# Optimization experiments

Measured on AMD Instinct MI355X. Metric: run time of the kernel, lower is better.

Reference implementation:

```python
import jax, jax.numpy as jnp
import numpy as np
import math

# Dimensions (see shape_source)
B, C, NH = 4, 256, 8
VP, VW = 6, 16   # vertical: patches-per-window (outer), windows (inner)
HP, HW = 32, 3   # horizontal: patches-per-window (outer), windows (inner)
NW, P = VW * HW, VP * HP   # 48 windows, 192 patches per window
GRID = 96                   # patch grid is 96x96
SHIFT = (HP // 2, VP // 2)  # (16, 3) = (window_shape[0]//2, window_shape[1]//2)
FF = 4 * C
SCALE = 1.0 / math.sqrt(C)  # source divides by sqrt(embedding_dim), not head_dim


def setup_inputs() -> dict:
    key = jax.random.key(0)
    ks = jax.random.split(key, 17)
    std = 0.02
    n = lambda k, s: (jax.random.normal(k, s, dtype=jnp.float32) * std)
    return {
        "embeddings": jax.random.normal(ks[0], (B, GRID, GRID, C), dtype=jnp.float32),
        "ln1_g": jnp.ones((C,), jnp.float32), "ln1_b": jnp.zeros((C,), jnp.float32),
        "wq": n(ks[1], (C, C)), "bq": jnp.zeros((C,), jnp.float32),
        "wk": n(ks[2], (C, C)), "bk": jnp.zeros((C,), jnp.float32),
        "wv": n(ks[3], (C, C)), "bv": jnp.zeros((C,), jnp.float32),
        "pos_bias": n(ks[4], (NH, P, P)),
        "ln2_g": jnp.ones((C,), jnp.float32), "ln2_b": jnp.zeros((C,), jnp.float32),
        "w1": n(ks[5], (C, FF)), "b1": jnp.zeros((FF,), jnp.float32),
        "w2": n(ks[6], (FF, C)), "b2": jnp.zeros((C,), jnp.float32),
    }


def _ln(x, g, b, eps=1e-5):
    m = jnp.mean(x, axis=-1, keepdims=True)
    v = jnp.mean(jnp.square(x - m), axis=-1, keepdims=True)
    return (x - m) * jax.lax.rsqrt(v + eps) * g + b


def reference(embeddings, ln1_g, ln1_b, wq, bq, wk, bk, wv, bv, pos_bias,
              ln2_g, ln2_b, w1, b1, w2, b2):
    x = jnp.roll(embeddings, SHIFT, axis=(1, 2))
    # part: H=(VP outer, VW inner), W=(HP outer, HW inner) -> [B, NW, P, C]
    p = x.reshape(B, VP, VW, HP, HW, C).transpose(0, 2, 4, 1, 3, 5).reshape(B, NW, P, C)
    y = _ln(p, ln1_g, ln1_b)
    def heads(w, b):
        return (y @ w + b).reshape(B, NW, P, NH, C // NH).transpose(0, 1, 3, 2, 4)
    q, k, v = heads(wq, bq), heads(wk, bk), heads(wv, bv)  # [B, NW, NH, P, Dh]
    logits = jnp.einsum('bwhpd,bwhqd->bwhpq', q, k) * SCALE + pos_bias
    attn = jax.nn.softmax(logits, axis=-1)
    sa = jnp.einsum('bwhpq,bwhqd->bwhpd', attn, v)
    sa = sa.transpose(0, 1, 3, 2, 4).reshape(B, NW, P, C)
    a = p + sa
    h = _ln(a, ln2_g, ln2_b)
    ff = jax.nn.gelu(h @ w1 + b1, approximate=False) @ w2 + b2
    out = a + ff
    # join: inverse of part
    o = out.reshape(B, VW, HW, VP, HP, C).transpose(0, 3, 1, 4, 2, 5).reshape(B, GRID, GRID, C)
    return jnp.roll(o, (-SHIFT[0], -SHIFT[1]), axis=(1, 2))
```

## Files before the change

### kernel.cpp

```cpp
#include <hip/hip_runtime.h>
#include <hip/hip_bf16.h>
#include <cstdint>

using bf16x8 = __attribute__((ext_vector_type(8))) short;
using f32x4  = __attribute__((ext_vector_type(4))) float;
using bf16_t = __hip_bfloat16;

#define DEVI static __device__ __forceinline__

constexpr int kB = 4, kC = 256, kNH = 8, kDh = 32;
constexpr int kVP = 6, kVW = 16, kHP = 32, kHW = 3;
constexpr int kNW = 48, kP = 192, kGRID = 96;
constexpr int kRows = kB * kNW * kP;
constexpr int kFF = 1024;
constexpr float kScale = 0.0625f;

DEVI void row_coords(int row, int& b, int& g1, int& g2) {
  int b_  = row / (kNW * kP);
  int rem = row - b_ * (kNW * kP);
  int w = rem / kP;
  int p = rem - w * kP;
  int vw = w / kHW, hw = w - vw * kHW;
  int vp = p >> 5,  hp = p & 31;
  int r  = vp * kVW + vw;
  int cc = hp * kHW + hw;
  g1 = r + 80;  if (g1 >= kGRID) g1 -= kGRID;
  g2 = cc + 93; if (g2 >= kGRID) g2 -= kGRID;
  b = b_;
}

DEVI float bf2f(short s) {
  union { unsigned u; float f; } c;
  c.u = ((unsigned)(unsigned short)s) << 16;
  return c.f;
}
DEVI short f2bf(float f) {
  bf16_t h = __float2bfloat16(f);
  return *reinterpret_cast<short*>(&h);
}

DEVI void gload16(const void* g, void* l) {
  __builtin_amdgcn_global_load_lds(
      (__attribute__((address_space(1))) void*)(uintptr_t)g,
      (__attribute__((address_space(3))) void*)(uintptr_t)l, 16, 0, 0);
}

DEVI bf16x8 ds_read_b128(uint32_t byte_off) {
  bf16x8 v;
  asm volatile("ds_read_b128 %0, %1" : "=v"(v) : "v"(byte_off));
  return v;
}

DEVI float gelu_fast(float v) {
  const float t2 = v * fmaf(0.0713548162f, v * v, 1.5957691216f);
  return v / (1.f + __expf(-t2));
}

__global__ __launch_bounds__(256) void k_wconv(
    const float* __restrict__ wq, const float* __restrict__ wk,
    const float* __restrict__ wv, const float* __restrict__ w1,
    const float* __restrict__ w2, bf16_t* __restrict__ W) {
  const int i = blockIdx.x * 256 + threadIdx.x;
  if (i < 196608) {
    const int n = i >> 8, k = i & 255;
    const float* src = n < 256 ? wq : (n < 512 ? wk : wv);
    W[i] = __float2bfloat16(src[k * 256 + (n & 255)]);
  } else if (i < 458752) {
    const int j = i - 196608;
    const int n = j >> 8, k = j & 255;
    W[i] = __float2bfloat16(w1[k * 1024 + n]);
  } else if (i < 720896) {
    const int j = i - 458752;
    const int n = j >> 10, k = j & 1023;
    W[i] = __float2bfloat16(w2[k * 256 + n]);
  }
}

__global__ __launch_bounds__(256) void k_ln1(const float* __restrict__ emb,
    const float* __restrict__ gam, const float* __restrict__ bet,
    bf16_t* __restrict__ Y) {
  const int wave = threadIdx.x >> 6, lane = threadIdx.x & 63;
  #pragma unroll
  for (int rr = 0; rr < 2; ++rr) {
    const int row = blockIdx.x * 8 + wave * 2 + rr;
    int b, g1, g2; row_coords(row, b, g1, g2);
    const float* src = emb + (((size_t)b * kGRID + g1) * kGRID + g2) * kC;
    float4 x = *reinterpret_cast<const float4*>(src + lane * 4);
    float s  = x.x + x.y + x.z + x.w;
    float sq = x.x*x.x + x.y*x.y + x.z*x.z + x.w*x.w;
    #pragma unroll
    for (int off = 32; off; off >>= 1) { s += __shfl_xor(s, off); sq += __shfl_xor(sq, off); }
    const float mean = s * (1.f / kC);
    const float rstd = rsqrtf(sq * (1.f / kC) - mean * mean + 1e-5f);
    const float4 g4 = *reinterpret_cast<const float4*>(gam + lane * 4);
    const float4 b4 = *reinterpret_cast<const float4*>(bet + lane * 4);
    short4 o;
    o.x = f2bf((x.x - mean) * rstd * g4.x + b4.x);
    o.y = f2bf((x.y - mean) * rstd * g4.y + b4.y);
    o.z = f2bf((x.z - mean) * rstd * g4.z + b4.z);
    o.w = f2bf((x.w - mean) * rstd * g4.w + b4.w);
    *reinterpret_cast<short4*>(Y + (size_t)row * kC + lane * 4) = o;
  }
}

__global__ __launch_bounds__(256) void k_ln2(const float* __restrict__ emb,
    const bf16_t* __restrict__ SA,
    const float* __restrict__ gam, const float* __restrict__ bet,
    bf16_t* __restrict__ A, bf16_t* __restrict__ H) {
  const int wave = threadIdx.x >> 6, lane = threadIdx.x & 63;
  #pragma unroll
  for (int rr = 0; rr < 2; ++rr) {
    const int row = blockIdx.x * 8 + wave * 2 + rr;
    int b, g1, g2; row_coords(row, b, g1, g2);
    const float* src = emb + (((size_t)b * kGRID + g1) * kGRID + g2) * kC;
    float4 x = *reinterpret_cast<const float4*>(src + lane * 4);
    short4 sv = *reinterpret_cast<const short4*>(SA + (size_t)row * kC + lane * 4);
    x.x += bf2f(sv.x); x.y += bf2f(sv.y); x.z += bf2f(sv.z); x.w += bf2f(sv.w);
    short4 av;
    av.x = f2bf(x.x); av.y = f2bf(x.y); av.z = f2bf(x.z); av.w = f2bf(x.w);
    *reinterpret_cast<short4*>(A + (size_t)row * kC + lane * 4) = av;
    float s  = x.x + x.y + x.z + x.w;
    float sq = x.x*x.x + x.y*x.y + x.z*x.z + x.w*x.w;
    #pragma unroll
    for (int off = 32; off; off >>= 1) { s += __shfl_xor(s, off); sq += __shfl_xor(sq, off); }
    const float mean = s * (1.f / kC);
    const float rstd = rsqrtf(sq * (1.f / kC) - mean * mean + 1e-5f);
    const float4 g4 = *reinterpret_cast<const float4*>(gam + lane * 4);
    const float4 b4 = *reinterpret_cast<const float4*>(bet + lane * 4);
    short4 o;
    o.x = f2bf((x.x - mean) * rstd * g4.x + b4.x);
    o.y = f2bf((x.y - mean) * rstd * g4.y + b4.y);
    o.z = f2bf((x.z - mean) * rstd * g4.z + b4.z);
    o.w = f2bf((x.w - mean) * rstd * g4.w + b4.w);
    *reinterpret_cast<short4*>(H + (size_t)row * kC + lane * 4) = o;
  }
}

template <int KDIM, int EPI, int GX>
__global__ __launch_bounds__(256, 3) void k_gemm8(
    const bf16_t* __restrict__ Amat, const bf16_t* __restrict__ BT,
    const float* __restrict__ bias0, const float* __restrict__ bias1,
    const float* __restrict__ bias2,
    bf16_t* __restrict__ Obf, const bf16_t* __restrict__ Ares,
    float* __restrict__ Out) {
  __shared__ short sm[24576];
  bf16_t* As[3] = {(bf16_t*)&sm[0], (bf16_t*)&sm[4096], (bf16_t*)&sm[8192]};
  bf16_t* Bs[3] = {(bf16_t*)&sm[12288], (bf16_t*)&sm[16384], (bf16_t*)&sm[20480]};
  const int tid = threadIdx.x;
  const int wave = tid >> 6, lane = tid & 63;
  const int lr = lane & 15, kg4 = lane >> 4;
  const int nwg = (kRows / 128) * GX;
  const int wg = (blockIdx.x & 7) * (nwg >> 3) + (blockIdx.x >> 3);
  const int m0 = (wg / GX) * 128, n0 = (wg % GX) * 128;
  const int wm = (wave >> 1) * 64, wn = (wave & 1) * 64;
  const int srow = lane >> 2;
  const int scol = ((lane & 3) ^ ((srow >> 1) & 3)) << 3;

  auto stage = [&](bf16_t* aDst, bf16_t* bDst, int k0) {
    #pragma unroll
    for (int i = 0; i < 2; ++i) {
      const int c = wave * 2 + i;
      const int row = c * 16 + srow;
      gload16(Amat + (size_t)(m0 + row) * KDIM + k0 + scol, aDst + c * 512);
      gload16(BT   + (size_t)(n0 + row) * KDIM + k0 + scol, bDst + c * 512);
    }
  };

  const uint32_t aOff[3] = {(uint32_t)(uintptr_t)As[0], (uint32_t)(uintptr_t)As[1],
                            (uint32_t)(uintptr_t)As[2]};
  const uint32_t bOff[3] = {(uint32_t)(uintptr_t)Bs[0], (uint32_t)(uintptr_t)Bs[1],
                            (uint32_t)(uintptr_t)Bs[2]};

  f32x4 acc[4][4] = {};
  auto compute = [&](uint32_t aBase, uint32_t bBase) {
    bf16x8 af[4], bq[4];
    #pragma unroll
    for (int m = 0; m < 4; ++m) {
      const int r = wm + m * 16 + lr;
      af[m] = ds_read_b128(aBase + r * 64 + ((kg4 ^ ((r >> 1) & 3)) << 4));
    }
    #pragma unroll
    for (int n = 0; n < 4; ++n) {
      const int r = wn + n * 16 + lr;
      bq[n] = ds_read_b128(bBase + r * 64 + ((kg4 ^ ((r >> 1) & 3)) << 4));
    }
    asm volatile("s_waitcnt lgkmcnt(0)" ::: "memory");
    __builtin_amdgcn_sched_barrier(0);
    __builtin_amdgcn_s_setprio(1);
    #pragma unroll
    for (int m = 0; m < 4; ++m)
      #pragma unroll
      for (int n = 0; n < 4; ++n)
        acc[m][n] = __builtin_amdgcn_mfma_f32_16x16x32_bf16(af[m], bq[n], acc[m][n], 0, 0, 0);
    __builtin_amdgcn_s_setprio(0);
  };

  stage(As[0], Bs[0], 0);
  if (KDIM > 32) stage(As[1], Bs[1], 32);
  constexpr int NT = KDIM / 32;
  #pragma unroll
  for (int t = 0; t < NT; ++t) {
    if (t + 1 < NT) {
      asm volatile("s_waitcnt vmcnt(4)" ::: "memory");
    } else {
      asm volatile("s_waitcnt vmcnt(0)" ::: "memory");
    }
    __builtin_amdgcn_sched_barrier(0);
    __builtin_amdgcn_s_barrier();
    if (t + 2 < NT)
      stage(As[(t + 2) % 3], Bs[(t + 2) % 3], (t + 2) * 32);
    compute(aOff[t % 3], bOff[t % 3]);
  }
  __builtin_amdgcn_s_barrier();
  __builtin_amdgcn_sched_barrier(0);

  if constexpr (EPI == 0 || EPI == 1) {
    short* scr = &sm[wave * 4096];
    const int colbase = n0 + wn;
    const float* bp;
    int cb;
    if constexpr (EPI == 0) {
      const int which = colbase >> 8;
      bp = which == 0 ? bias0 : (which == 1 ? bias1 : bias2);
      cb = colbase & 255;
    } else { bp = bias0; cb = colbase; }
    #pragma unroll
    for (int m = 0; m < 4; ++m)
      #pragma unroll
      for (int n = 0; n < 4; ++n)
        #pragma unroll
        for (int r = 0; r < 4; ++r) {
          const int lrow = m * 16 + kg4 * 4 + r;
          const int lcol = n * 16 + lr;
          float v = acc[m][n][r] + bp[cb + lcol];
          if constexpr (EPI == 1) v = gelu_fast(v);
          scr[lrow * 64 + (lcol ^ (((lrow >> 2) & 3) << 4))] = f2bf(v);
        }
    const int rl = lane >> 3, cl = (lane & 7) * 8;
    bf16_t* const obase = (EPI == 0)
        ? Obf + (size_t)(colbase >> 8) * kRows * kC
        : Obf;
    const int ld = (EPI == 0) ? kC : kFF;
    #pragma unroll
    for (int p = 0; p < 8; ++p) {
      const int lrow = p * 8 + rl;
      bf16x8 v = *reinterpret_cast<const bf16x8*>(
          &scr[lrow * 64 + (cl ^ (((lrow >> 2) & 3) << 4))]);
      *reinterpret_cast<bf16x8*>(
          obase + (size_t)(m0 + wm + lrow) * ld + cb + cl) = v;
    }
  } else {
    float* scrf = reinterpret_cast<float*>(&sm[wave * 4096]);
    #pragma unroll
    for (int h = 0; h < 2; ++h) {
      #pragma unroll
      for (int m = 0; m < 4; ++m)
        #pragma unroll
        for (int nn = 0; nn < 2; ++nn) {
          const int n = h * 2 + nn;
          #pragma unroll
          for (int r = 0; r < 4; ++r) {
            const int lrow = m * 16 + kg4 * 4 + r;
            const int lcol = nn * 16 + lr;
            scrf[lrow * 32 + (lcol ^ (((lrow >> 2) & 3) << 3))] =
                acc[m][n][r] + bias0[n0 + wn + n * 16 + lr];
          }
        }
      const int rl = lane >> 3, cl = (lane & 7) * 4;
      #pragma unroll
      for (int p = 0; p < 8; ++p) {
        const int lrow = p * 8 + rl;
        const int row = m0 + wm + lrow;
        const int col = n0 + wn + h * 32 + cl;
        float4 v = *reinterpret_cast<const float4*>(
            &scrf[lrow * 32 + (cl ^ (((lrow >> 2) & 3) << 3))]);
        const short4 a4 = *reinterpret_cast<const short4*>(
            &Ares[(size_t)row * kC + col]);
        v.x += bf2f(a4.x); v.y += bf2f(a4.y);
        v.z += bf2f(a4.z); v.w += bf2f(a4.w);
        int b, g1, g2; row_coords(row, b, g1, g2);
        *reinterpret_cast<float4*>(
            &Out[(((size_t)b * kGRID + g1) * kGRID + g2) * kC + col]) = v;
      }
      if (h == 0) __builtin_amdgcn_s_barrier();
    }
  }
}

constexpr int kKsPad = 40;
constexpr int kVtPad = 200;
constexpr int kPlPad = 200;
__global__ __launch_bounds__(256) void k_attn(
    const bf16_t* __restrict__ Q, const bf16_t* __restrict__ K,
    const bf16_t* __restrict__ V, const float* __restrict__ pos,
    bf16_t* __restrict__ SA) {
  __shared__ short Ks[kP * kKsPad];
  __shared__ short Vt[kDh * kVtPad];
  __shared__ short Pl[4 * 16 * kPlPad];
  const int bw = blockIdx.x >> 3, h = blockIdx.x & 7;
  const int rowbase = bw * kP, colbase = h * kDh;
  const int tid = threadIdx.x, wave = tid >> 6, lane = tid & 63;
  const int lr = lane & 15, kg = lane >> 4;
  const int wq0 = wave * 48;
  const float* pb = pos + (size_t)h * kP * kP;

  #pragma unroll
  for (int i = 0; i < 3; ++i) {
    const int c = tid + i * 256;
    const int row = c >> 2, dch = (c & 3) * 8;
    const size_t gbase = (size_t)(rowbase + row) * kC + colbase + dch;
    bf16x8 kv = *reinterpret_cast<const bf16x8*>(K + gbase);
    *reinterpret_cast<bf16x8*>(&Ks[row * kKsPad + dch]) = kv;
    bf16x8 vv = *reinterpret_cast<const bf16x8*>(V + gbase);
    #pragma unroll
    for (int e = 0; e < 8; ++e) Vt[(dch + e) * kVtPad + row] = vv[e];
  }
  __syncthreads();

  for (int m = 0; m < 3; ++m) {
    const int rbase = wq0 + m * 16;
    bf16x8 aq = *reinterpret_cast<const bf16x8*>(
        Q + (size_t)(rowbase + rbase + lr) * kC + colbase + kg * 8);
    f32x4 s[12];
    #pragma unroll
    for (int n = 0; n < 12; ++n) {
      bf16x8 bk = *reinterpret_cast<const bf16x8*>(&Ks[(n * 16 + lr) * kKsPad + kg * 8]);
      s[n] = __builtin_amdgcn_mfma_f32_16x16x32_bf16(aq, bk, (f32x4){0.f, 0.f, 0.f, 0.f}, 0, 0, 0);
    }
    float mx[4] = {-1e30f, -1e30f, -1e30f, -1e30f};
    #pragma unroll
    for (int n = 0; n < 12; ++n) {
      #pragma unroll
      for (int r = 0; r < 4; ++r) {
        const float lg = fmaf(s[n][r], kScale,
                              pb[(size_t)(rbase + kg * 4 + r) * kP + n * 16 + lr]);
        s[n][r] = lg;
        mx[r] = fmaxf(mx[r], lg);
      }
    }
    #pragma unroll
    for (int r = 0; r < 4; ++r)
      #pragma unroll
      for (int off = 8; off; off >>= 1) mx[r] = fmaxf(mx[r], __shfl_xor(mx[r], off));
    float sm4[4] = {0.f, 0.f, 0.f, 0.f};
    #pragma unroll
    for (int n = 0; n < 12; ++n)
      #pragma unroll
      for (int r = 0; r < 4; ++r) {
        const float e = __expf(s[n][r] - mx[r]);
        s[n][r] = e;
        sm4[r] += e;
      }
    #pragma unroll
    for (int r = 0; r < 4; ++r) {
      #pragma unroll
      for (int off = 8; off; off >>= 1) sm4[r] += __shfl_xor(sm4[r], off);
      sm4[r] = 1.f / sm4[r];
    }
    #pragma unroll
    for (int n = 0; n < 12; ++n)
      #pragma unroll
      for (int r = 0; r < 4; ++r)
        Pl[(wave * 16 + kg * 4 + r) * kPlPad + n * 16 + lr] = f2bf(s[n][r] * sm4[r]);
    f32x4 o0 = {0.f, 0.f, 0.f, 0.f}, o1 = {0.f, 0.f, 0.f, 0.f};
    #pragma unroll
    for (int kk = 0; kk < 6; ++kk) {
      bf16x8 ap = *reinterpret_cast<const bf16x8*>(&Pl[(wave * 16 + lr) * kPlPad + kk * 32 + kg * 8]);
      bf16x8 b0 = *reinterpret_cast<const bf16x8*>(&Vt[lr * kVtPad + kk * 32 + kg * 8]);
      bf16x8 b1 = *reinterpret_cast<const bf16x8*>(&Vt[(16 + lr) * kVtPad + kk * 32 + kg * 8]);
      o0 = __builtin_amdgcn_mfma_f32_16x16x32_bf16(ap, b0, o0, 0, 0, 0);
      o1 = __builtin_amdgcn_mfma_f32_16x16x32_bf16(ap, b1, o1, 0, 0, 0);
    }
    short* scr2 = &Pl[wave * 16 * kPlPad];
    #pragma unroll
    for (int r = 0; r < 4; ++r) {
      scr2[(kg * 4 + r) * 32 + lr]      = f2bf(o0[r]);
      scr2[(kg * 4 + r) * 32 + 16 + lr] = f2bf(o1[r]);
    }
    {
      const int rrow = lane >> 2, c0 = (lane & 3) * 8;
      bf16x8 v = *reinterpret_cast<const bf16x8*>(&scr2[rrow * 32 + c0]);
      *reinterpret_cast<bf16x8*>(
          SA + (size_t)(rowbase + rbase + rrow) * kC + colbase + c0) = v;
    }
  }
}

extern "C" void kernel_launch(void* const* d_in, const int* in_sizes, int n_in,
                              void* d_out, int out_size, void* d_ws, size_t ws_size,
                              hipStream_t stream) {
  const float* emb  = (const float*)d_in[0];
  const float* ln1g = (const float*)d_in[1];
  const float* ln1b = (const float*)d_in[2];
  const float* wq   = (const float*)d_in[3];
  const float* bq   = (const float*)d_in[4];
  const float* wk   = (const float*)d_in[5];
  const float* bk   = (const float*)d_in[6];
  const float* wv   = (const float*)d_in[7];
  const float* bv   = (const float*)d_in[8];
  const float* pos  = (const float*)d_in[9];
  const float* ln2g = (const float*)d_in[10];
  const float* ln2b = (const float*)d_in[11];
  const float* w1   = (const float*)d_in[12];
  const float* b1   = (const float*)d_in[13];
  const float* w2   = (const float*)d_in[14];
  const float* b2   = (const float*)d_in[15];

  char* ws = (char*)d_ws;
  const size_t nYb = (size_t)kRows * kC * 2;
  bf16_t* Y    = (bf16_t*)(ws);
  bf16_t* Qb   = (bf16_t*)(ws + nYb);
  bf16_t* SAb  = (bf16_t*)(ws + nYb * 4);
  bf16_t* Abuf = (bf16_t*)(ws + nYb * 5);
  bf16_t* H    = (bf16_t*)(ws + nYb * 5 + (size_t)kRows * kC * 4);
  bf16_t* G    = (bf16_t*)(ws);
  bf16_t* W    = (bf16_t*)(ws + nYb * 5 + (size_t)kRows * kC * 4 + nYb);
  bf16_t* WqkvT = W;
  bf16_t* W1T   = W + 768 * 256;
  bf16_t* W2T   = W1T + 1024 * 256;

  k_wconv<<<2816, 256, 0, stream>>>(wq, wk, wv, w1, w2, W);
  k_ln1<<<kRows / 8, 256, 0, stream>>>(emb, ln1g, ln1b, Y);
  k_gemm8<256, 0, 6><<<(kRows / 128) * 6, 256, 0, stream>>>(
      Y, WqkvT, bq, bk, bv, Qb, nullptr, nullptr);
  k_attn<<<kB * kNW * kNH, 256, 0, stream>>>(
      Qb, Qb + (size_t)kRows * kC, Qb + 2 * (size_t)kRows * kC, pos, SAb);
  k_ln2<<<kRows / 8, 256, 0, stream>>>(emb, SAb, ln2g, ln2b, Abuf, H);
  k_gemm8<256, 1, 8><<<(kRows / 128) * 8, 256, 0, stream>>>(
      H, W1T, b1, nullptr, nullptr, G, nullptr, nullptr);
  k_gemm8<1024, 2, 2><<<(kRows / 128) * 2, 256, 0, stream>>>(
      G, W2T, b2, nullptr, nullptr, nullptr, Abuf, (float*)d_out);
}
```

Baseline: 171.1 us.

## Use 256x128 GEMM tiles for QKV and FFN1 to double B-tile reuse

```diff
diff --git a/kernel.cpp b/kernel.cpp
--- a/kernel.cpp
+++ b/kernel.cpp
@@ -137,52 +137,50 @@
 }
 
 template <int KDIM, int EPI, int GX>
-__global__ __launch_bounds__(256, 3) void k_gemm8(
+__global__ __launch_bounds__(256, 2) void k_gemm9(
     const bf16_t* __restrict__ Amat, const bf16_t* __restrict__ BT,
     const float* __restrict__ bias0, const float* __restrict__ bias1,
     const float* __restrict__ bias2,
-    bf16_t* __restrict__ Obf, const bf16_t* __restrict__ Ares,
-    float* __restrict__ Out) {
-  __shared__ short sm[24576];
-  bf16_t* As[3] = {(bf16_t*)&sm[0], (bf16_t*)&sm[4096], (bf16_t*)&sm[8192]};
-  bf16_t* Bs[3] = {(bf16_t*)&sm[12288], (bf16_t*)&sm[16384], (bf16_t*)&sm[20480]};
+    bf16_t* __restrict__ Obf) {
+  __shared__ short sm[36864];
   const int tid = threadIdx.x;
   const int wave = tid >> 6, lane = tid & 63;
   const int lr = lane & 15, kg4 = lane >> 4;
-  const int nwg = (kRows / 128) * GX;
+  const int nwg = (kRows / 256) * GX;
   const int wg = (blockIdx.x & 7) * (nwg >> 3) + (blockIdx.x >> 3);
-  const int m0 = (wg / GX) * 128, n0 = (wg % GX) * 128;
+  const int m0 = (wg / GX) * 256, n0 = (wg % GX) * 128;
   const int wm = (wave >> 1) * 64, wn = (wave & 1) * 64;
   const int srow = lane >> 2;
   const int scol = ((lane & 3) ^ ((srow >> 1) & 3)) << 3;
 
-  auto stage = [&](bf16_t* aDst, bf16_t* bDst, int k0) {
+  auto stage = [&](int buf, int k0) {
+    bf16_t* const base = (bf16_t*)&sm[buf * 12288];
     #pragma unroll
     for (int i = 0; i < 2; ++i) {
       const int c = wave * 2 + i;
       const int row = c * 16 + srow;
-      gload16(Amat + (size_t)(m0 + row) * KDIM + k0 + scol, aDst + c * 512);
-      gload16(BT   + (size_t)(n0 + row) * KDIM + k0 + scol, bDst + c * 512);
+      gload16(Amat + (size_t)(m0 + row) * KDIM + k0 + scol, base + c * 512);
+      gload16(Amat + (size_t)(m0 + 128 + row) * KDIM + k0 + scol,
+              base + 4096 + c * 512);
+      gload16(BT + (size_t)(n0 + row) * KDIM + k0 + scol, base + 8192 + c * 512);
     }
   };
 
-  const uint32_t aOff[3] = {(uint32_t)(uintptr_t)As[0], (uint32_t)(uintptr_t)As[1],
-                            (uint32_t)(uintptr_t)As[2]};
-  const uint32_t bOff[3] = {(uint32_t)(uintptr_t)Bs[0], (uint32_t)(uintptr_t)Bs[1],
-                            (uint32_t)(uintptr_t)Bs[2]};
-
-  f32x4 acc[4][4] = {};
-  auto compute = [&](uint32_t aBase, uint32_t bBase) {
-    bf16x8 af[4], bq[4];
+  f32x4 acc0[4][4] = {}, acc1[4][4] = {};
+  auto compute = [&](int buf) {
+    const uint32_t base = (uint32_t)(uintptr_t)&sm[buf * 12288];
+    bf16x8 bq[4], a0[4], a1[4];
+    #pragma unroll
+    for (int n = 0; n < 4; ++n) {
+      const int r = wn + n * 16 + lr;
+      bq[n] = ds_read_b128(base + 16384 + r * 64 + ((kg4 ^ ((r >> 1) & 3)) << 4));
+    }
     #pragma unroll
     for (int m = 0; m < 4; ++m) {
       const int r = wm + m * 16 + lr;
-      af[m] = ds_read_b128(aBase + r * 64 + ((kg4 ^ ((r >> 1) & 3)) << 4));
-    }
-    #pragma unroll
-    for (int n = 0; n < 4; ++n) {
-      const int r = wn + n * 16 + lr;
-      bq[n] = ds_read_b128(bBase + r * 64 + ((kg4 ^ ((r >> 1) & 3)) << 4));
+      const uint32_t off = r * 64 + ((kg4 ^ ((r >> 1) & 3)) << 4);
+      a0[m] = ds_read_b128(base + off);
+      a1[m] = ds_read_b128(base + 8192 + off);
     }
     asm volatile("s_waitcnt lgkmcnt(0)" ::: "memory");
     __builtin_amdgcn_sched_barrier(0);
@@ -191,30 +189,34 @@
     for (int m = 0; m < 4; ++m)
       #pragma unroll
       for (int n = 0; n < 4; ++n)
-        acc[m][n] = __builtin_amdgcn_mfma_f32_16x16x32_bf16(af[m], bq[n], acc[m][n], 0, 0, 0);
+        acc0[m][n] = __builtin_amdgcn_mfma_f32_16x16x32_bf16(a0[m], bq[n], acc0[m][n], 0, 0, 0);
+    #pragma unroll
+    for (int m = 0; m < 4; ++m)
+      #pragma unroll
+      for (int n = 0; n < 4; ++n)
+        acc1[m][n] = __builtin_amdgcn_mfma_f32_16x16x32_bf16(a1[m], bq[n], acc1[m][n], 0, 0, 0);
     __builtin_amdgcn_s_setprio(0);
   };
 
-  stage(As[0], Bs[0], 0);
-  if (KDIM > 32) stage(As[1], Bs[1], 32);
+  stage(0, 0);
+  if (KDIM > 32) stage(1, 32);
   constexpr int NT = KDIM / 32;
   #pragma unroll
   for (int t = 0; t < NT; ++t) {
     if (t + 1 < NT) {
-      asm volatile("s_waitcnt vmcnt(4)" ::: "memory");
+      asm volatile("s_waitcnt vmcnt(6)" ::: "memory");
     } else {
       asm volatile("s_waitcnt vmcnt(0)" ::: "memory");
     }
     __builtin_amdgcn_sched_barrier(0);
     __builtin_amdgcn_s_barrier();
-    if (t + 2 < NT)
-      stage(As[(t + 2) % 3], Bs[(t + 2) % 3], (t + 2) * 32);
-    compute(aOff[t % 3], bOff[t % 3]);
+    if (t + 2 < NT) stage((t + 2) % 3, (t + 2) * 32);
+    compute(t % 3);
   }
   __builtin_amdgcn_s_barrier();
   __builtin_amdgcn_sched_barrier(0);
 
-  if constexpr (EPI == 0 || EPI == 1) {
+  auto epi = [&](const f32x4 (&acc)[4][4], int mbase) {
     short* scr = &sm[wave * 4096];
     const int colbase = n0 + wn;
     const float* bp;
@@ -247,43 +249,122 @@
       bf16x8 v = *reinterpret_cast<const bf16x8*>(
           &scr[lrow * 64 + (cl ^ (((lrow >> 2) & 3) << 4))]);
       *reinterpret_cast<bf16x8*>(
-          obase + (size_t)(m0 + wm + lrow) * ld + cb + cl) = v;
-    }
-  } else {
-    float* scrf = reinterpret_cast<float*>(&sm[wave * 4096]);
-    #pragma unroll
-    for (int h = 0; h < 2; ++h) {
-      #pragma unroll
-      for (int m = 0; m < 4; ++m)
+          obase + (size_t)(mbase + wm + lrow) * ld + cb + cl) = v;
+    }
+  };
+  epi(acc0, m0);
+  epi(acc1, m0 + 128);
+}
+
+template <int KDIM, int GX>
+__global__ __launch_bounds__(256, 3) void k_gemm8(
+    const bf16_t* __restrict__ Amat, const bf16_t* __restrict__ BT,
+    const float* __restrict__ bias0, const bf16_t* __restrict__ Ares,
+    float* __restrict__ Out) {
+  __shared__ short sm[24576];
+  bf16_t* As[3] = {(bf16_t*)&sm[0], (bf16_t*)&sm[4096], (bf16_t*)&sm[8192]};
+  bf16_t* Bs[3] = {(bf16_t*)&sm[12288], (bf16_t*)&sm[16384], (bf16_t*)&sm[20480]};
+  const int tid = threadIdx.x;
+  const int wave = tid >> 6, lane = tid & 63;
+  const int lr = lane & 15, kg4 = lane >> 4;
+  const int nwg = (kRows / 128) * GX;
+  const int wg = (blockIdx.x & 7) * (nwg >> 3) + (blockIdx.x >> 3);
+  const int m0 = (wg / GX) * 128, n0 = (wg % GX) * 128;
+  const int wm = (wave >> 1) * 64, wn = (wave & 1) * 64;
+  const int srow = lane >> 2;
+  const int scol = ((lane & 3) ^ ((srow >> 1) & 3)) << 3;
+
+  auto stage = [&](bf16_t* aDst, bf16_t* bDst, int k0) {
+    #pragma unroll
+    for (int i = 0; i < 2; ++i) {
+      const int c = wave * 2 + i;
+      const int row = c * 16 + srow;
+      gload16(Amat + (size_t)(m0 + row) * KDIM + k0 + scol, aDst + c * 512);
+      gload16(BT   + (size_t)(n0 + row) * KDIM + k0 + scol, bDst + c * 512);
+    }
+  };
+
+  const uint32_t aOff[3] = {(uint32_t)(uintptr_t)As[0], (uint32_t)(uintptr_t)As[1],
+                            (uint32_t)(uintptr_t)As[2]};
+  const uint32_t bOff[3] = {(uint32_t)(uintptr_t)Bs[0], (uint32_t)(uintptr_t)Bs[1],
+                            (uint32_t)(uintptr_t)Bs[2]};
+
+  f32x4 acc[4][4] = {};
+  auto compute = [&](uint32_t aBase, uint32_t bBase) {
+    bf16x8 af[4], bq[4];
+    #pragma unroll
+    for (int m = 0; m < 4; ++m) {
+      const int r = wm + m * 16 + lr;
+      af[m] = ds_read_b128(aBase + r * 64 + ((kg4 ^ ((r >> 1) & 3)) << 4));
+    }
+    #pragma unroll
+    for (int n = 0; n < 4; ++n) {
+      const int r = wn + n * 16 + lr;
+      bq[n] = ds_read_b128(bBase + r * 64 + ((kg4 ^ ((r >> 1) & 3)) << 4));
+    }
+    asm volatile("s_waitcnt lgkmcnt(0)" ::: "memory");
+    __builtin_amdgcn_sched_barrier(0);
+    __builtin_amdgcn_s_setprio(1);
+    #pragma unroll
+    for (int m = 0; m < 4; ++m)
+      #pragma unroll
+      for (int n = 0; n < 4; ++n)
+        acc[m][n] = __builtin_amdgcn_mfma_f32_16x16x32_bf16(af[m], bq[n], acc[m][n], 0, 0, 0);
+    __builtin_amdgcn_s_setprio(0);
+  };
+
+  stage(As[0], Bs[0], 0);
+  stage(As[1], Bs[1], 32);
+  constexpr int NT = KDIM / 32;
+  #pragma unroll
+  for (int t = 0; t < NT; ++t) {
+    if (t + 1 < NT) {
+      asm volatile("s_waitcnt vmcnt(4)" ::: "memory");
+    } else {
+      asm volatile("s_waitcnt vmcnt(0)" ::: "memory");
+    }
+    __builtin_amdgcn_sched_barrier(0);
+    __builtin_amdgcn_s_barrier();
+    if (t + 2 < NT)
+      stage(As[(t + 2) % 3], Bs[(t + 2) % 3], (t + 2) * 32);
+    compute(aOff[t % 3], bOff[t % 3]);
+  }
+  __builtin_amdgcn_s_barrier();
+  __builtin_amdgcn_sched_barrier(0);
+
+  float* scrf = reinterpret_cast<float*>(&sm[wave * 4096]);
+  #pragma unroll
+  for (int h = 0; h < 2; ++h) {
+    #pragma unroll
+    for (int m = 0; m < 4; ++m)
+      #pragma unroll
+      for (int nn = 0; nn < 2; ++nn) {
+        const int n = h * 2 + nn;
         #pragma unroll
-        for (int nn = 0; nn < 2; ++nn) {
-          const int n = h * 2 + nn;
-          #pragma unroll
-          for (int r = 0; r < 4; ++r) {
-            const int lrow = m * 16 + kg4 * 4 + r;
-            const int lcol = nn * 16 + lr;
-            scrf[lrow * 32 + (lcol ^ (((lrow >> 2) & 3) << 3))] =
-                acc[m][n][r] + bias0[n0 + wn + n * 16 + lr];
-          }
+        for (int r = 0; r < 4; ++r) {
+          const int lrow = m * 16 + kg4 * 4 + r;
+          const int lcol = nn * 16 + lr;
+          scrf[lrow * 32 + (lcol ^ (((lrow >> 2) & 3) << 3))] =
+              acc[m][n][r] + bias0[n0 + wn + n * 16 + lr];
         }
-      const int rl = lane >> 3, cl = (lane & 7) * 4;
-      #pragma unroll
-      for (int p = 0; p < 8; ++p) {
-        const int lrow = p * 8 + rl;
-        const int row = m0 + wm + lrow;
-        const int col = n0 + wn + h * 32 + cl;
-        float4 v = *reinterpret_cast<const float4*>(
-            &scrf[lrow * 32 + (cl ^ (((lrow >> 2) & 3) << 3))]);
-        const short4 a4 = *reinterpret_cast<const short4*>(
-            &Ares[(size_t)row * kC + col]);
-        v.x += bf2f(a4.x); v.y += bf2f(a4.y);
-        v.z += bf2f(a4.z); v.w += bf2f(a4.w);
-        int b, g1, g2; row_coords(row, b, g1, g2);
-        *reinterpret_cast<float4*>(
-            &Out[(((size_t)b * kGRID + g1) * kGRID + g2) * kC + col]) = v;
       }
-      if (h == 0) __builtin_amdgcn_s_barrier();
-    }
+    const int rl = lane >> 3, cl = (lane & 7) * 4;
+    #pragma unroll
+    for (int p = 0; p < 8; ++p) {
+      const int lrow = p * 8 + rl;
+      const int row = m0 + wm + lrow;
+      const int col = n0 + wn + h * 32 + cl;
+      float4 v = *reinterpret_cast<const float4*>(
+          &scrf[lrow * 32 + (cl ^ (((lrow >> 2) & 3) << 3))]);
+      const short4 a4 = *reinterpret_cast<const short4*>(
+          &Ares[(size_t)row * kC + col]);
+      v.x += bf2f(a4.x); v.y += bf2f(a4.y);
+      v.z += bf2f(a4.z); v.w += bf2f(a4.w);
+      int b, g1, g2; row_coords(row, b, g1, g2);
+      *reinterpret_cast<float4*>(
+          &Out[(((size_t)b * kGRID + g1) * kGRID + g2) * kC + col]) = v;
+    }
+    if (h == 0) __builtin_amdgcn_s_barrier();
   }
 }
 
@@ -421,13 +502,13 @@
 
   k_wconv<<<2816, 256, 0, stream>>>(wq, wk, wv, w1, w2, W);
   k_ln1<<<kRows / 8, 256, 0, stream>>>(emb, ln1g, ln1b, Y);
-  k_gemm8<256, 0, 6><<<(kRows / 128) * 6, 256, 0, stream>>>(
-      Y, WqkvT, bq, bk, bv, Qb, nullptr, nullptr);
+  k_gemm9<256, 0, 6><<<(kRows / 256) * 6, 256, 0, stream>>>(
+      Y, WqkvT, bq, bk, bv, Qb);
   k_attn<<<kB * kNW * kNH, 256, 0, stream>>>(
       Qb, Qb + (size_t)kRows * kC, Qb + 2 * (size_t)kRows * kC, pos, SAb);
   k_ln2<<<kRows / 8, 256, 0, stream>>>(emb, SAb, ln2g, ln2b, Abuf, H);
-  k_gemm8<256, 1, 8><<<(kRows / 128) * 8, 256, 0, stream>>>(
-      H, W1T, b1, nullptr, nullptr, G, nullptr, nullptr);
-  k_gemm8<1024, 2, 2><<<(kRows / 128) * 2, 256, 0, stream>>>(
-      G, W2T, b2, nullptr, nullptr, nullptr, Abuf, (float*)d_out);
-}
+  k_gemm9<256, 1, 8><<<(kRows / 256) * 8, 256, 0, stream>>>(
+      H, W1T, b1, nullptr, nullptr, G);
+  k_gemm8<1024, 2><<<(kRows / 128) * 2, 256, 0, stream>>>(
+      G, W2T, b2, Abuf, (float*)d_out);
+}
```

After: 182.4 us. +6.6%, slower.
